# Kernel tuning notes

Measured on AMD Instinct MI355X. Metric: run time of the kernel, lower is better.

The kernel has to match this reference:

```python
import jax, jax.numpy as jnp
import numpy as np

N = 512 * 512
E = N * 8


def setup_inputs() -> dict:
    key = jax.random.key(0)
    ks = jax.random.split(key, 20)
    inp = {
        "x": jax.random.normal(ks[0], (N, 4), dtype=jnp.float32),
        "edge_src": jax.random.randint(ks[1], (E,), 0, N, dtype=jnp.int32),
        "edge_dst": jax.random.randint(ks[2], (E,), 0, N, dtype=jnp.int32),
        "grid_size": 512,
        # GCN linear weights (PyG GCNConv: lin has no bias; separate bias added after aggregation)
        "W1": jax.random.normal(ks[3], (4, 64), dtype=jnp.float32) * 0.5,
        "b1": jnp.zeros((64,), dtype=jnp.float32),
        "W2": jax.random.normal(ks[4], (64, 64), dtype=jnp.float32) * 0.125,
        "b2": jnp.zeros((64,), dtype=jnp.float32),
        "W3": jax.random.normal(ks[5], (64, 64), dtype=jnp.float32) * 0.125,
        "b3": jnp.zeros((64,), dtype=jnp.float32),
        # CNN stack (OIHW)
        "cw1": jax.random.normal(ks[6], (32, 64, 3, 3), dtype=jnp.float32) * 0.04,
        "cb1": jnp.zeros((32,), dtype=jnp.float32),
        "cw2": jax.random.normal(ks[7], (16, 32, 3, 3), dtype=jnp.float32) * 0.06,
        "cb2": jnp.zeros((16,), dtype=jnp.float32),
        "cw3": jax.random.normal(ks[8], (8, 16, 3, 3), dtype=jnp.float32) * 0.08,
        "cb3": jnp.zeros((8,), dtype=jnp.float32),
        "cw4": jax.random.normal(ks[9], (6, 8, 3, 3), dtype=jnp.float32) * 0.12,
        "cb4": jnp.zeros((6,), dtype=jnp.float32),
    }
    return inp


def _conv(x, w, b):
    # x: [1, C, H, W], w: [O, I, 3, 3]
    y = jax.lax.conv_general_dilated(x, w, (1, 1), 'SAME',
                                     dimension_numbers=('NCHW', 'OIHW', 'NCHW'))
    return y + b[None, :, None, None]


def reference(x, edge_src, edge_dst, grid_size, W1, b1, W2, b2, W3, b3,
              cw1, cb1, cw2, cb2, cw3, cb3, cw4, cb4):
    n = x.shape[0]
    loops = jnp.arange(n, dtype=edge_src.dtype)
    src = jnp.concatenate([edge_src, loops])  # message source j
    dst = jnp.concatenate([edge_dst, loops])  # aggregation target i
    ones = jnp.ones(src.shape[0], dtype=x.dtype)
    deg = jax.ops.segment_sum(ones, dst, num_segments=n)
    dinv = jnp.where(deg > 0, jax.lax.rsqrt(deg), 0.0)
    norm = (dinv[src] * dinv[dst])[:, None]  # [E+N, 1]

    def gcn(h, W, b):
        h = h @ W
        msg = h[src] * norm
        agg = jax.ops.segment_sum(msg, dst, num_segments=n)
        return agg + b

    h = jax.nn.relu(gcn(x, W1, b1))
    h = jax.nn.relu(gcn(h, W2, b2))
    h = jax.nn.relu(gcn(h, W3, b3))

    # [N, 64] -> [1, grid, grid, 64] -> [1, 64, grid, grid]
    img = h.reshape(1, grid_size, grid_size, -1).transpose(0, 3, 1, 2)
    y = jax.nn.relu(_conv(img, cw1, cb1))
    y = jax.nn.relu(_conv(y, cw2, cb2))
    y = jax.nn.relu(_conv(y, cw3, cb3))
    y = _conv(y, cw4, cb4)
    return y[0]  # [6, grid, grid]
```

## Files before the change

kernel.cpp:

```cpp
#include <hip/hip_runtime.h>

#define NN 262144
#define NE 2097152
constexpr int GS = 512;
constexpr int P  = GS * GS;
constexpr int BSTRIDE = 12288;
constexpr int PADP = 1024;

typedef __attribute__((ext_vector_type(16))) float f32x16;
typedef __attribute__((ext_vector_type(8)))  float f32x8;
typedef __attribute__((ext_vector_type(4)))  float f32x4;
typedef __attribute__((ext_vector_type(2)))  float f32x2;
typedef __attribute__((ext_vector_type(8)))  short s16x8;

__device__ __forceinline__ unsigned short f2bf(float f) {
  unsigned u = __float_as_uint(f);
  return (unsigned short)((u + 0x7FFF + ((u >> 16) & 1)) >> 16);
}
__device__ __forceinline__ float bf2f(unsigned short h) {
  return __uint_as_float((unsigned)h << 16);
}

template <int N> struct WFull;
template <> struct WFull<8> {
  f32x16 v0, v1, v2, v3; f32x8 v4;
  __device__ __forceinline__ void load(const float* p) {
    asm volatile(
      "s_load_dwordx16 %0, %5, 0x0\n\t"
      "s_load_dwordx16 %1, %5, 0x40\n\t"
      "s_load_dwordx16 %2, %5, 0x80\n\t"
      "s_load_dwordx16 %3, %5, 0xc0\n\t"
      "s_load_dwordx8  %4, %5, 0x100\n\t"
      "s_waitcnt lgkmcnt(0)"
      : "=&s"(v0), "=&s"(v1), "=&s"(v2), "=&s"(v3), "=&s"(v4)
      : "s"(p));
  }
  __device__ __forceinline__ float get(int i) const {
    return i < 16 ? v0[i] : i < 32 ? v1[i - 16] : i < 48 ? v2[i - 32]
         : i < 64 ? v3[i - 48] : v4[i - 64];
  }
};
template <> struct WFull<6> {
  f32x16 v0, v1, v2; f32x4 v3; f32x2 v4;
  __device__ __forceinline__ void load(const float* p) {
    asm volatile(
      "s_load_dwordx16 %0, %5, 0x0\n\t"
      "s_load_dwordx16 %1, %5, 0x40\n\t"
      "s_load_dwordx16 %2, %5, 0x80\n\t"
      "s_load_dwordx4  %3, %5, 0xc0\n\t"
      "s_load_dwordx2  %4, %5, 0xd0\n\t"
      "s_waitcnt lgkmcnt(0)"
      : "=&s"(v0), "=&s"(v1), "=&s"(v2), "=&s"(v3), "=&s"(v4)
      : "s"(p));
  }
  __device__ __forceinline__ float get(int i) const {
    return i < 16 ? v0[i] : i < 32 ? v1[i - 16] : i < 48 ? v2[i - 32]
         : i < 52 ? v3[i - 48] : v4[i - 52];
  }
};

__global__ __launch_bounds__(256) void k_bhist(const int4* __restrict__ dst,
                                               int* __restrict__ gb) {
  __shared__ int lc[256];
  int t = threadIdx.x;
  lc[t] = 0;
  __syncthreads();
  int base = blockIdx.x * 1024;
#pragma unroll
  for (int q = 0; q < 4; ++q) {
    int4 d = dst[base + q * 256 + t];
    atomicAdd(&lc[d.x >> 10], 1); atomicAdd(&lc[d.y >> 10], 1);
    atomicAdd(&lc[d.z >> 10], 1); atomicAdd(&lc[d.w >> 10], 1);
  }
  __syncthreads();
  atomicAdd(&gb[t], lc[t]);
}

__global__ __launch_bounds__(256) void k_bscan(const int* __restrict__ gb,
                                               int* __restrict__ bbase,
                                               int* __restrict__ bcur) {
  __shared__ int sd[256];
  int t = threadIdx.x;
  sd[t] = gb[t];
  __syncthreads();
  for (int off = 1; off < 256; off <<= 1) {
    int v = (t >= off) ? sd[t - off] : 0;
    __syncthreads();
    sd[t] += v;
    __syncthreads();
  }
  int ex = (t == 0) ? 0 : sd[t - 1];
  bbase[t] = ex;
  bcur[t]  = ex;
  if (t == 255) bbase[256] = sd[255];
}

__global__ __launch_bounds__(256) void k_bin(const int4* __restrict__ src4,
                                             const int4* __restrict__ dst4,
                                             int* __restrict__ bcur,
                                             unsigned* __restrict__ pairs) {
  __shared__ int lcnt[256], lofs[256], lcur[256];
  __shared__ unsigned lp[4096];
  int t = threadIdx.x;
  lcnt[t] = 0;
  __syncthreads();
  int base = blockIdx.x * 1024;
  int4 dreg[4], sreg[4];
#pragma unroll
  for (int q = 0; q < 4; ++q) {
    dreg[q] = dst4[base + q * 256 + t];
    sreg[q] = src4[base + q * 256 + t];
  }
#pragma unroll
  for (int q = 0; q < 4; ++q) {
    atomicAdd(&lcnt[dreg[q].x >> 10], 1); atomicAdd(&lcnt[dreg[q].y >> 10], 1);
    atomicAdd(&lcnt[dreg[q].z >> 10], 1); atomicAdd(&lcnt[dreg[q].w >> 10], 1);
  }
  __syncthreads();
  int c = lcnt[t];
  lofs[t] = c;
  __syncthreads();
  for (int off = 1; off < 256; off <<= 1) {
    int v = (t >= off) ? lofs[t - off] : 0;
    __syncthreads();
    lofs[t] += v;
    __syncthreads();
  }
  int myofs = lofs[t] - c;
  lcur[t] = myofs;
  int gb = atomicAdd(&bcur[t], c);
  __syncthreads();
#pragma unroll
  for (int q = 0; q < 4; ++q) {
    int d[4] = {dreg[q].x, dreg[q].y, dreg[q].z, dreg[q].w};
    int s[4] = {sreg[q].x, sreg[q].y, sreg[q].z, sreg[q].w};
#pragma unroll
    for (int j = 0; j < 4; ++j) {
      int pos = atomicAdd(&lcur[d[j] >> 10], 1);
      lp[pos] = ((unsigned)(d[j] & 1023) << 18) | (unsigned)s[j];
    }
  }
  __syncthreads();
  for (int k = 0; k < c; ++k) pairs[gb + k] = lp[myofs + k];
}

__global__ __launch_bounds__(256) void k_bsort(const unsigned* __restrict__ pairs,
                                               const int* __restrict__ bbase,
                                               int* __restrict__ ssrc,
                                               int* __restrict__ offs,
                                               int* __restrict__ dgr,
                                               float* __restrict__ dinv) {
  __shared__ int cnt[1024], ofs[1024], sblk[256];
  int b = blockIdx.x, t = threadIdx.x;
  int s0 = bbase[b], n = bbase[b + 1] - s0;
  int gbase = b * BSTRIDE;
  for (int i = t; i < 1024; i += 256) cnt[i] = 0;
  __syncthreads();
  for (int i = t; i < n; i += 256) {
    unsigned p = pairs[s0 + i];
    atomicAdd(&cnt[p >> 18], 1);
  }
  __syncthreads();
  int l4 = t * 4;
  int c0 = cnt[l4], c1 = cnt[l4 + 1], c2 = cnt[l4 + 2], c3 = cnt[l4 + 3];
  int a0 = (c0 + 3) & ~3, a1 = (c1 + 3) & ~3, a2 = (c2 + 3) & ~3, a3 = (c3 + 3) & ~3;
  int sum = a0 + a1 + a2 + a3;
  sblk[t] = sum;
  __syncthreads();
  for (int off = 1; off < 256; off <<= 1) {
    int v = (t >= off) ? sblk[t - off] : 0;
    __syncthreads();
    sblk[t] += v;
    __syncthreads();
  }
  int ex = sblk[t] - sum;
  int o0 = gbase + ex, o1 = o0 + a0, o2 = o1 + a1, o3 = o2 + a2;
  ofs[l4] = o0; ofs[l4 + 1] = o1; ofs[l4 + 2] = o2; ofs[l4 + 3] = o3;
  int node = b * 1024 + l4;
  *(int4*)&offs[node] = make_int4(o0, o1, o2, o3);
  *(int4*)&dgr[node]  = make_int4(c0, c1, c2, c3);
  *(float4*)&dinv[node] = make_float4(rsqrtf((float)(c0 + 1)),
                                      rsqrtf((float)(c1 + 1)),
                                      rsqrtf((float)(c2 + 1)),
                                      rsqrtf((float)(c3 + 1)));
  for (int p = c0; p < a0; ++p) ssrc[o0 + p] = NN;
  for (int p = c1; p < a1; ++p) ssrc[o1 + p] = NN;
  for (int p = c2; p < a2; ++p) ssrc[o2 + p] = NN;
  for (int p = c3; p < a3; ++p) ssrc[o3 + p] = NN;
  __syncthreads();
  for (int i = t; i < n; i += 256) {
    unsigned p = pairs[s0 + i];
    int pos = atomicAdd(&ofs[p >> 18], 1);
    ssrc[pos] = (int)(p & 0x3FFFFu);
  }
}

__global__ void k_zrows(float* hA, float* hB, float* xs) {
  int t = threadIdx.x;
  if (t < 64) hA[(size_t)NN * 64 + t] = 0.f;
  else if (t < 128) hB[(size_t)NN * 64 + (t - 64)] = 0.f;
  else if (t < 132) xs[(size_t)NN * 4 + (t - 128)] = 0.f;
}

__global__ __launch_bounds__(256) void k_xscale(const float4* __restrict__ x,
                                                const float* __restrict__ dinv,
                                                float4* __restrict__ xs) {
  int i = blockIdx.x * 256 + threadIdx.x;
  float4 v = x[i];
  float d = dinv[i];
  xs[i] = make_float4(v.x * d, v.y * d, v.z * d, v.w * d);
}

__global__ __launch_bounds__(256) void k_agg4(const float4* __restrict__ xs,
                                              const float* __restrict__ dinv,
                                              const int* __restrict__ offs,
                                              const int* __restrict__ dgr,
                                              const int4* __restrict__ ssrc4,
                                              float4* __restrict__ out) {
  for (int i = blockIdx.x * 256 + threadIdx.x; i < NN; i += gridDim.x * 256) {
    float di = dinv[i];
    int k4 = offs[i] >> 2, deg = dgr[i];
    float4 acc = xs[i];
    int t4n = (deg + 3) >> 2;
    int4 s4 = ssrc4[k4];
    for (int t4 = 0; t4 < t4n; ++t4) {
      int4 nx = ssrc4[k4 + t4 + 1];
      float4 v0 = xs[s4.x], v1 = xs[s4.y], v2 = xs[s4.z], v3 = xs[s4.w];
      acc.x += v0.x + v1.x + v2.x + v3.x;
      acc.y += v0.y + v1.y + v2.y + v3.y;
      acc.z += v0.z + v1.z + v2.z + v3.z;
      acc.w += v0.w + v1.w + v2.w + v3.w;
      s4 = nx;
    }
    out[i] = make_float4(acc.x * di, acc.y * di, acc.z * di, acc.w * di);
  }
}

__global__ __launch_bounds__(256) void k_matmul4(const float* __restrict__ h,
                                                 const float* __restrict__ W,
                                                 const float* __restrict__ bias,
                                                 const float* __restrict__ dinv,
                                                 float* __restrict__ out) {
  int lane = threadIdx.x & 63;
  int wv   = threadIdx.x >> 6;
  float w0 = W[lane], w1 = W[64 + lane], w2 = W[128 + lane], w3 = W[192 + lane];
  float bl = bias[lane];
  for (int node = blockIdx.x * 4 + wv; node < NN; node += gridDim.x * 4) {
    float4 hv = *(const float4*)(h + (size_t)node * 4);
    float dn = dinv[node];
    float acc = fmaf(hv.x, w0, fmaf(hv.y, w1, fmaf(hv.z, w2, fmaf(hv.w, w3, bl))));
    out[(size_t)node * 64 + lane] = fmaxf(acc, 0.f) * dn;
  }
}

template <bool SCALE_OUT, bool BF16OUT>
__global__ __launch_bounds__(256) void k_aggW(const float* __restrict__ h,
                                              const float* __restrict__ dinv,
                                              const int* __restrict__ offs,
                                              const int* __restrict__ dgr,
                                              const int4* __restrict__ ssrc4,
                                              const float* __restrict__ W,
                                              const float* __restrict__ bias,
                                              float* __restrict__ out,
                                              unsigned short* __restrict__ xhi,
                                              unsigned short* __restrict__ xlo) {
  __shared__ float g[16][64];
  const float4* h4 = (const float4*)h;
  int lane = threadIdx.x & 63;
  int wv   = threadIdx.x >> 6;
  int sub  = lane >> 4;
  int fl   = lane & 15;
  float wreg[64];
#pragma unroll
  for (int k = 0; k < 64; ++k) wreg[k] = W[(size_t)k * 64 + lane];
  float bl = bias[lane];

  for (int i0 = (blockIdx.x * 4 + wv) * 4; i0 < NN; i0 += gridDim.x * 16) {
    int i = i0 + sub;
    float di = dinv[i];
    int k4 = offs[i] >> 2;
    int deg = dgr[i];
    int t4n = (deg + 3) >> 2;

    float4 acc  = h4[(size_t)i * 16 + fl];
    float4 accB = make_float4(0.f, 0.f, 0.f, 0.f);
    int4 sA = ssrc4[k4];
    int t4 = 0;
#pragma unroll 1
    for (; t4 + 2 <= t4n; t4 += 2) {
      int4 sB = ssrc4[k4 + t4 + 1];
      int4 nx = ssrc4[k4 + t4 + 2];
      float4 v0 = h4[(size_t)sA.x * 16 + fl];
      float4 v1 = h4[(size_t)sA.y * 16 + fl];
      float4 v2 = h4[(size_t)sA.z * 16 + fl];
      float4 v3 = h4[(size_t)sA.w * 16 + fl];
      float4 u0 = h4[(size_t)sB.x * 16 + fl];
      float4 u1 = h4[(size_t)sB.y * 16 + fl];
      float4 u2 = h4[(size_t)sB.z * 16 + fl];
      float4 u3 = h4[(size_t)sB.w * 16 + fl];
      acc.x  += v0.x + v1.x + v2.x + v3.x;
      acc.y  += v0.y + v1.y + v2.y + v3.y;
      acc.z  += v0.z + v1.z + v2.z + v3.z;
      acc.w  += v0.w + v1.w + v2.w + v3.w;
      accB.x += u0.x + u1.x + u2.x + u3.x;
      accB.y += u0.y + u1.y + u2.y + u3.y;
      accB.z += u0.z + u1.z + u2.z + u3.z;
      accB.w += u0.w + u1.w + u2.w + u3.w;
      sA = nx;
    }
    if (t4 < t4n) {
      float4 v0 = h4[(size_t)sA.x * 16 + fl];
      float4 v1 = h4[(size_t)sA.y * 16 + fl];
      float4 v2 = h4[(size_t)sA.z * 16 + fl];
      float4 v3 = h4[(size_t)sA.w * 16 + fl];
      acc.x += v0.x + v1.x + v2.x + v3.x;
      acc.y += v0.y + v1.y + v2.y + v3.y;
      acc.z += v0.z + v1.z + v2.z + v3.z;
      acc.w += v0.w + v1.w + v2.w + v3.w;
    }
    acc.x += accB.x; acc.y += accB.y; acc.z += accB.z; acc.w += accB.w;

    float4 sacc = make_float4(acc.x * di, acc.y * di, acc.z * di, acc.w * di);
    int row = wv * 4 + sub;
    *(float4*)&g[row][fl * 4] = sacc;
    asm volatile("s_waitcnt lgkmcnt(0)" ::: "memory");

#pragma unroll
    for (int n = 0; n < 4; ++n) {
      const float4* gp = (const float4*)&g[wv * 4 + n][0];
      float o = bl;
#pragma unroll
      for (int q = 0; q < 16; ++q) {
        float4 gv = gp[q];
        o = fmaf(gv.x, wreg[q * 4 + 0], o);
        o = fmaf(gv.y, wreg[q * 4 + 1], o);
        o = fmaf(gv.z, wreg[q * 4 + 2], o);
        o = fmaf(gv.w, wreg[q * 4 + 3], o);
      }
      float val = fmaxf(o, 0.f);
      if constexpr (SCALE_OUT) val *= dinv[i0 + n];
      if constexpr (BF16OUT) {
        size_t b = (size_t)(PADP + i0 + n) * 64 + lane;
        unsigned short hh = f2bf(val);
        xhi[b] = hh;
        xlo[b] = f2bf(val - bf2f(hh));
      } else {
        out[(size_t)(i0 + n) * 64 + lane] = val;
      }
    }
  }
}

__global__ __launch_bounds__(256) void k_wrepm(const float* __restrict__ w,
                                               unsigned short* __restrict__ whim,
                                               unsigned short* __restrict__ wlom) {
  int idx = blockIdx.x * 256 + threadIdx.x;
  if (idx >= 9 * 2 * 2 * 512) return;
  int i  = idx & 7;
  int l  = (idx >> 3) & 63;
  int nf = (idx >> 9) & 1;
  int ks = (idx >> 10) & 1;
  int t  = idx >> 11;
  int o = nf * 16 + (l & 15);
  int c = ks * 32 + (l >> 4) * 8 + i;
  float v = w[(o * 64 + c) * 9 + t];
  unsigned short h = f2bf(v);
  whim[idx] = h;
  wlom[idx] = f2bf(v - bf2f(h));
}

__global__ __launch_bounds__(256) void k_conv1m(const unsigned short* __restrict__ xhi,
                                                const unsigned short* __restrict__ xlo,
                                                const unsigned short* __restrict__ whim,
                                                const unsigned short* __restrict__ wlom,
                                                const float* __restrict__ cb,
                                                float* __restrict__ outp) {
  constexpr int PXS  = 80;
  constexpr int ROWB = 66 * PXS;
  constexpr int HALF = 6 * ROWB;
  __shared__ __align__(16) unsigned char smem[2 * HALF];

  int tid  = threadIdx.x;
  int lane = tid & 63, wv = tid >> 6;
  int sx = blockIdx.x & 7, gy = blockIdx.x >> 3;
  int x0 = sx * 64, y0 = gy * 4;
  int lm = lane & 15, lc = lane >> 4;

  f32x4 acc[4][2];
#pragma unroll
  for (int mf = 0; mf < 4; ++mf)
#pragma unroll
    for (int nf = 0; nf < 2; ++nf) acc[mf][nf] = (f32x4){0.f, 0.f, 0.f, 0.f};

#pragma unroll 1
  for (int ks = 0; ks < 2; ++ks) {
    if (ks) __syncthreads();
#pragma unroll 1
    for (int it = 0; it < 13; ++it) {
      int idx = it * 256 + tid;
      if (idx < 3168) {
        int arr = idx >= 1584;
        int rem = arr ? idx - 1584 : idx;
        int chunk = rem & 3;
        int pxr = rem >> 2;
        int r = pxr / 66, px = pxr - r * 66;
        int xx = x0 - 1 + px;
        uint4 v = make_uint4(0u, 0u, 0u, 0u);
        if (xx >= 0 && xx < GS) {
          size_t p = (size_t)(PADP + (y0 - 1 + r) * GS + xx);
          const unsigned short* src = arr ? xlo : xhi;
          v = *(const uint4*)((const unsigned char*)src + p * 128 + ks * 64 + chunk * 16);
        }
        *(uint4*)(smem + arr * HALF + r * ROWB + px * PXS + chunk * 16) = v;
      }
    }
    __syncthreads();
#pragma unroll 1
    for (int t = 0; t < 9; ++t) {
      int ky = t / 3, kx = t % 3;
      const unsigned short* wb = whim + (size_t)(((t * 2 + ks) * 2) * 64 + lane) * 8;
      const unsigned short* wl = wlom + (size_t)(((t * 2 + ks) * 2) * 64 + lane) * 8;
      s16x8 bh0 = *(const s16x8*)(wb);
      s16x8 bh1 = *(const s16x8*)(wb + 512);
      s16x8 bl0 = *(const s16x8*)(wl);
      s16x8 bl1 = *(const s16x8*)(wl + 512);
      int r = wv + ky;
#pragma unroll
      for (int mf = 0; mf < 4; ++mf) {
        int px = mf * 16 + lm + kx;
        const unsigned char* ap = smem + r * ROWB + px * PXS + lc * 16;
        s16x8 ah = *(const s16x8*)(ap);
        s16x8 al = *(const s16x8*)(ap + HALF);
        acc[mf][0] = __builtin_amdgcn_mfma_f32_16x16x32_bf16(ah, bh0, acc[mf][0], 0, 0, 0);
        acc[mf][0] = __builtin_amdgcn_mfma_f32_16x16x32_bf16(ah, bl0, acc[mf][0], 0, 0, 0);
        acc[mf][0] = __builtin_amdgcn_mfma_f32_16x16x32_bf16(al, bh0, acc[mf][0], 0, 0, 0);
        acc[mf][1] = __builtin_amdgcn_mfma_f32_16x16x32_bf16(ah, bh1, acc[mf][1], 0, 0, 0);
        acc[mf][1] = __builtin_amdgcn_mfma_f32_16x16x32_bf16(ah, bl1, acc[mf][1], 0, 0, 0);
        acc[mf][1] = __builtin_amdgcn_mfma_f32_16x16x32_bf16(al, bh1, acc[mf][1], 0, 0, 0);
      }
    }
  }
  __syncthreads();

  float* lds = (float*)smem;
#pragma unroll
  for (int mf = 0; mf < 4; ++mf)
#pragma unroll
    for (int nf = 0; nf < 2; ++nf)
#pragma unroll
      for (int r = 0; r < 4; ++r)
        lds[((wv * 64 + mf * 16 + lc * 4 + r) * 33) + nf * 16 + lm] = acc[mf][nf][r];
  asm volatile("s_waitcnt lgkmcnt(0)" ::: "memory");

  size_t ob = (size_t)(y0 + wv) * GS + x0 + lane;
#pragma unroll
  for (int o = 0; o < 32; ++o) {
    float v = lds[((wv * 64 + lane) * 33) + o] + cb[o];
    outp[(size_t)o * P + ob] = fmaxf(v, 0.f);
  }
}

template <int CIN, int COUT, int COUTB>
__global__ __launch_bounds__(256) void k_wrep(const float* __restrict__ w,
                                              float* __restrict__ wr) {
  int i = blockIdx.x * 256 + threadIdx.x;
  if (i >= CIN * 9 * COUT) return;
  int ol = i % COUTB;
  int t  = (i / COUTB) % 9;
  int c  = (i / (COUTB * 9)) % CIN;
  int g  = i / (COUTB * 9 * CIN);
  wr[i] = w[(((g * COUTB + ol) * CIN) + c) * 9 + t];
}

template <int CIN, int COUTB, bool RELU>
__global__ __launch_bounds__(256) void k_conv(const float* __restrict__ in,
                                              const float* __restrict__ wrep,
                                              const float* __restrict__ cb,
                                              float* __restrict__ out) {
  int tx = threadIdx.x;
  int ty = threadIdx.y;
  int g  = blockIdx.z;
  int x0 = (blockIdx.x * 64 + tx) * 2;
  int y  = blockIdx.y * 4 + ty;

  float acc0[COUTB], acc1[COUTB];
#pragma unroll
  for (int o = 0; o < COUTB; ++o) { acc0[o] = 0.f; acc1[o] = 0.f; }

  bool xlo = x0 > 0;
  bool xhi = x0 < GS - 2;
  int rok[3], yoff[3];
#pragma unroll
  for (int r = 0; r < 3; ++r) {
    int yy = y + r - 1;
    rok[r] = (yy >= 0) && (yy < GS);
    int yc = yy < 0 ? 0 : (yy > GS - 1 ? GS - 1 : yy);
    yoff[r] = yc * GS;
  }
  const float* wg = wrep + (size_t)g * CIN * 9 * COUTB;

  WFull<COUTB> w;
#pragma unroll 1
  for (int c = 0; c < CIN; ++c) {
    float iv[3][4];
#pragma unroll
    for (int r = 0; r < 3; ++r) {
      const float* ip = in + (size_t)c * P + yoff[r] + x0;
      if (rok[r]) {
        float2 m = *(const float2*)ip;
        iv[r][1] = m.x; iv[r][2] = m.y;
        iv[r][0] = xlo ? ip[-1] : 0.f;
        iv[r][3] = xhi ? ip[2]  : 0.f;
      } else {
        iv[r][0] = iv[r][1] = iv[r][2] = iv[r][3] = 0.f;
      }
    }
    w.load(wg + (size_t)c * 9 * COUTB);
#pragma unroll
    for (int t9 = 0; t9 < 9; ++t9) {
      int ky = t9 / 3, kx = t9 % 3;
      float a = iv[ky][kx], b2 = iv[ky][kx + 1];
#pragma unroll
      for (int o = 0; o < COUTB; ++o) {
        float wv = w.get(t9 * COUTB + o);
        acc0[o] = fmaf(a, wv, acc0[o]);
        acc1[o] = fmaf(b2, wv, acc1[o]);
      }
    }
  }

  size_t obase = (size_t)(g * COUTB) * P + (size_t)y * GS + x0;
#pragma unroll
  for (int o = 0; o < COUTB; ++o) {
    float bv = cb[g * COUTB + o];
    float v0 = acc0[o] + bv;
    float v1 = acc1[o] + bv;
    if (RELU) { v0 = fmaxf(v0, 0.f); v1 = fmaxf(v1, 0.f); }
    *(float2*)&out[obase + (size_t)o * P] = make_float2(v0, v1);
  }
}

extern "C" void kernel_launch(void* const* d_in, const int* in_sizes, int n_in,
                              void* d_out, int out_size, void* d_ws, size_t ws_size,
                              hipStream_t stream) {
  const float* x   = (const float*)d_in[0];
  const int*   esr = (const int*)d_in[1];
  const int*   eds = (const int*)d_in[2];
  const float* W1  = (const float*)d_in[4];
  const float* b1  = (const float*)d_in[5];
  const float* W2  = (const float*)d_in[6];
  const float* b2  = (const float*)d_in[7];
  const float* W3  = (const float*)d_in[8];
  const float* b3  = (const float*)d_in[9];
  const float* cw1 = (const float*)d_in[10];
  const float* cb1 = (const float*)d_in[11];
  const float* cw2 = (const float*)d_in[12];
  const float* cb2 = (const float*)d_in[13];
  const float* cw3 = (const float*)d_in[14];
  const float* cb3 = (const float*)d_in[15];
  const float* cw4 = (const float*)d_in[16];
  const float* cb4 = (const float*)d_in[17];
  float* out = (float*)d_out;

  char* ws = (char*)d_ws;
  const size_t MB = 1 << 20;
  const size_t KB = 1 << 10;
  const size_t XBYTES = (size_t)(P + 2 * PADP) * 64 * 2;
  unsigned*        pairs = (unsigned*)(ws);
  float*           xs    = (float*)(ws);
  float*           hA    = (float*)(ws);
  unsigned short*  xhi   = (unsigned short*)(ws);
  unsigned short*  xlo   = (unsigned short*)(ws + XBYTES);
  float*           cA    = (float*)(ws);
  float*           xagg  = (float*)(ws + 65 * MB);
  float*           hB    = (float*)(ws + 65 * MB);
  float*           cB    = (float*)(ws + 65 * MB);
  int*             ssrc  = (int*)(ws + 130 * MB);
  float*           dinv  = (float*)(ws + 142 * MB + 8 * KB);
  int*             dgr   = (int*)(ws + 143 * MB + 16 * KB);
  int*             offs  = (int*)(ws + 144 * MB + 24 * KB);
  int*             gb    = (int*)(ws + 145 * MB + 32 * KB);
  int*             bbase = (int*)(ws + 145 * MB + 36 * KB);
  int*             bcur  = (int*)(ws + 145 * MB + 40 * KB);
  unsigned short*  whim  = (unsigned short*)(ws + 145 * MB + 48 * KB);
  unsigned short*  wlom  = (unsigned short*)(ws + 145 * MB + 88 * KB);
  float*           wr2   = (float*)(ws + 145 * MB + 128 * KB);
  float*           wr3   = wr2 + 32 * 9 * 16;
  float*           wr4   = wr3 + 16 * 9 * 8;

  k_wrepm<<<72, 256, 0, stream>>>(cw1, whim, wlom);
  k_wrep<32, 16, 8><<<(32 * 9 * 16 + 255) / 256, 256, 0, stream>>>(cw2, wr2);
  k_wrep<16,  8, 8><<<(16 * 9 *  8 + 255) / 256, 256, 0, stream>>>(cw3, wr3);
  k_wrep< 8,  6, 6><<<( 8 * 9 *  6 + 255) / 256, 256, 0, stream>>>(cw4, wr4);

  hipMemsetAsync(gb, 0, 256 * sizeof(int), stream);
  k_bhist<<<512, 256, 0, stream>>>((const int4*)eds, gb);
  k_bscan<<<1, 256, 0, stream>>>(gb, bbase, bcur);
  k_bin<<<512, 256, 0, stream>>>((const int4*)esr, (const int4*)eds, bcur, pairs);
  k_bsort<<<256, 256, 0, stream>>>(pairs, bbase, ssrc, offs, dgr, dinv);

  k_zrows<<<1, 256, 0, stream>>>(hA, hB, xs);
  k_xscale<<<NN / 256, 256, 0, stream>>>((const float4*)x, dinv, (float4*)xs);
  k_agg4<<<1024, 256, 0, stream>>>((const float4*)xs, dinv, offs, dgr,
                                   (const int4*)ssrc, (float4*)xagg);
  k_matmul4<<<2048, 256, 0, stream>>>(xagg, W1, b1, dinv, hA);
  k_aggW<true, false><<<2048, 256, 0, stream>>>(hA, dinv, offs, dgr,
                                                (const int4*)ssrc, W2, b2, hB,
                                                nullptr, nullptr);
  const size_t PADB = (size_t)PADP * 64 * 2;
  hipMemsetAsync((char*)xhi, 0, PADB, stream);
  hipMemsetAsync((char*)xhi + (size_t)(PADP + P) * 128, 0, PADB, stream);
  hipMemsetAsync((char*)xlo, 0, PADB, stream);
  hipMemsetAsync((char*)xlo + (size_t)(PADP + P) * 128, 0, PADB, stream);
  k_aggW<false, true><<<2048, 256, 0, stream>>>(hB, dinv, offs, dgr,
                                                (const int4*)ssrc, W3, b3, hB,
                                                xhi, xlo);

  k_conv1m<<<1024, 256, 0, stream>>>(xhi, xlo, whim, wlom, cb1, cB);
  k_conv<32, 8, true ><<<dim3(4, 128, 2), dim3(64, 4), 0, stream>>>(cB, wr2, cb2, cA);
  k_conv<16, 8, true ><<<dim3(4, 128, 1), dim3(64, 4), 0, stream>>>(cA, wr3, cb3, cB);
  k_conv< 8, 6, false><<<dim3(4, 128, 1), dim3(64, 4), 0, stream>>>(cB, wr4, cb4, out);
}
```

Baseline: 427.2 us.

## Run conv2 on MFMA with split-bf16 NHWC output from conv1

Conv1 now writes its ReLU output as pixel-major hi/lo bf16 pairs instead of planar fp32. A new MFMA-based conv2 kernel reads this layout through LDS tiles and uses three bf16 MFMAs per tile to approximate fp32 accuracy, replacing the scalar fp32 conv for the 32→16 layer. This aims to cut the FP32 ALU cost of conv2 and the fp32 intermediate traffic. In exchange it adds padding memsets and relies on split-bf16 precision.

```diff
diff --git a/kernel.cpp b/kernel.cpp
--- a/kernel.cpp
+++ b/kernel.cpp
@@ -6,6 +6,7 @@
 constexpr int P  = GS * GS;
 constexpr int BSTRIDE = 12288;
 constexpr int PADP = 1024;
+constexpr int PADP2 = 1024;
 
 typedef __attribute__((ext_vector_type(16))) float f32x16;
 typedef __attribute__((ext_vector_type(8)))  float f32x8;
@@ -369,12 +370,29 @@
   wlom[idx] = f2bf(v - bf2f(h));
 }
 
+__global__ __launch_bounds__(256) void k_wrepm2(const float* __restrict__ w,
+                                                unsigned short* __restrict__ whim,
+                                                unsigned short* __restrict__ wlom) {
+  int idx = blockIdx.x * 256 + threadIdx.x;
+  if (idx >= 9 * 512) return;
+  int i = idx & 7;
+  int l = (idx >> 3) & 63;
+  int t = idx >> 9;
+  int o = l & 15;
+  int c = (l >> 4) * 8 + i;
+  float v = w[(o * 32 + c) * 9 + t];
+  unsigned short h = f2bf(v);
+  whim[idx] = h;
+  wlom[idx] = f2bf(v - bf2f(h));
+}
+
 __global__ __launch_bounds__(256) void k_conv1m(const unsigned short* __restrict__ xhi,
                                                 const unsigned short* __restrict__ xlo,
                                                 const unsigned short* __restrict__ whim,
                                                 const unsigned short* __restrict__ wlom,
                                                 const float* __restrict__ cb,
-                                                float* __restrict__ outp) {
+                                                unsigned short* __restrict__ y2hi,
+                                                unsigned short* __restrict__ y2lo) {
   constexpr int PXS  = 80;
   constexpr int ROWB = 66 * PXS;
   constexpr int HALF = 6 * ROWB;
@@ -452,10 +470,98 @@
         lds[((wv * 64 + mf * 16 + lc * 4 + r) * 33) + nf * 16 + lm] = acc[mf][nf][r];
   asm volatile("s_waitcnt lgkmcnt(0)" ::: "memory");
 
+  size_t pp = (size_t)PADP2 + (size_t)(y0 + wv) * GS + x0 + lane;
+  unsigned uh[16], ul[16];
+#pragma unroll
+  for (int o2 = 0; o2 < 16; ++o2) {
+    float v0 = fmaxf(lds[(wv * 64 + lane) * 33 + 2 * o2]     + cb[2 * o2],     0.f);
+    float v1 = fmaxf(lds[(wv * 64 + lane) * 33 + 2 * o2 + 1] + cb[2 * o2 + 1], 0.f);
+    unsigned short h0 = f2bf(v0), h1 = f2bf(v1);
+    unsigned short l0 = f2bf(v0 - bf2f(h0)), l1 = f2bf(v1 - bf2f(h1));
+    uh[o2] = (unsigned)h0 | ((unsigned)h1 << 16);
+    ul[o2] = (unsigned)l0 | ((unsigned)l1 << 16);
+  }
+  uint4* dh = (uint4*)(y2hi + pp * 32);
+  uint4* dl = (uint4*)(y2lo + pp * 32);
+#pragma unroll
+  for (int q = 0; q < 4; ++q) {
+    dh[q] = make_uint4(uh[q * 4], uh[q * 4 + 1], uh[q * 4 + 2], uh[q * 4 + 3]);
+    dl[q] = make_uint4(ul[q * 4], ul[q * 4 + 1], ul[q * 4 + 2], ul[q * 4 + 3]);
+  }
+}
+
+__global__ __launch_bounds__(256) void k_conv2m(const unsigned short* __restrict__ y2hi,
+                                                const unsigned short* __restrict__ y2lo,
+                                                const unsigned short* __restrict__ whim,
+                                                const unsigned short* __restrict__ wlom,
+                                                const float* __restrict__ cb,
+                                                float* __restrict__ outp) {
+  constexpr int PXS  = 80;
+  constexpr int ROWB = 66 * PXS;
+  constexpr int HALF = 6 * ROWB;
+  __shared__ __align__(16) unsigned char smem[2 * HALF];
+
+  int tid  = threadIdx.x;
+  int lane = tid & 63, wv = tid >> 6;
+  int sx = blockIdx.x & 7, gy = blockIdx.x >> 3;
+  int x0 = sx * 64, y0 = gy * 4;
+  int lm = lane & 15, lc = lane >> 4;
+
+  f32x4 acc[4];
+#pragma unroll
+  for (int mf = 0; mf < 4; ++mf) acc[mf] = (f32x4){0.f, 0.f, 0.f, 0.f};
+
+#pragma unroll 1
+  for (int it = 0; it < 13; ++it) {
+    int idx = it * 256 + tid;
+    if (idx < 3168) {
+      int arr = idx >= 1584;
+      int rem = arr ? idx - 1584 : idx;
+      int chunk = rem & 3;
+      int pxr = rem >> 2;
+      int r = pxr / 66, px = pxr - r * 66;
+      int xx = x0 - 1 + px;
+      uint4 v = make_uint4(0u, 0u, 0u, 0u);
+      if (xx >= 0 && xx < GS) {
+        size_t p = (size_t)(PADP2 + (y0 - 1 + r) * GS + xx);
+        const unsigned short* src = arr ? y2lo : y2hi;
+        v = *(const uint4*)((const unsigned char*)src + p * 64 + chunk * 16);
+      }
+      *(uint4*)(smem + arr * HALF + r * ROWB + px * PXS + chunk * 16) = v;
+    }
+  }
+  __syncthreads();
+#pragma unroll 1
+  for (int t = 0; t < 9; ++t) {
+    int ky = t / 3, kx = t % 3;
+    s16x8 bh = *(const s16x8*)(whim + ((size_t)t * 64 + lane) * 8);
+    s16x8 bl = *(const s16x8*)(wlom + ((size_t)t * 64 + lane) * 8);
+    int r = wv + ky;
+#pragma unroll
+    for (int mf = 0; mf < 4; ++mf) {
+      int px = mf * 16 + lm + kx;
+      const unsigned char* ap = smem + r * ROWB + px * PXS + lc * 16;
+      s16x8 ah = *(const s16x8*)(ap);
+      s16x8 al = *(const s16x8*)(ap + HALF);
+      acc[mf] = __builtin_amdgcn_mfma_f32_16x16x32_bf16(ah, bh, acc[mf], 0, 0, 0);
+      acc[mf] = __builtin_amdgcn_mfma_f32_16x16x32_bf16(ah, bl, acc[mf], 0, 0, 0);
+      acc[mf] = __builtin_amdgcn_mfma_f32_16x16x32_bf16(al, bh, acc[mf], 0, 0, 0);
+    }
+  }
+  __syncthreads();
+
+  float* lds = (float*)smem;
+#pragma unroll
+  for (int mf = 0; mf < 4; ++mf)
+#pragma unroll
+    for (int r = 0; r < 4; ++r)
+      lds[((wv * 64 + mf * 16 + lc * 4 + r) * 17) + lm] = acc[mf][r];
+  asm volatile("s_waitcnt lgkmcnt(0)" ::: "memory");
+
   size_t ob = (size_t)(y0 + wv) * GS + x0 + lane;
 #pragma unroll
-  for (int o = 0; o < 32; ++o) {
-    float v = lds[((wv * 64 + lane) * 33) + o] + cb[o];
+  for (int o = 0; o < 16; ++o) {
+    float v = lds[((wv * 64 + lane) * 17) + o] + cb[o];
     outp[(size_t)o * P + ob] = fmaxf(v, 0.f);
   }
 }
@@ -574,7 +680,9 @@
   float*           cA    = (float*)(ws);
   float*           xagg  = (float*)(ws + 65 * MB);
   float*           hB    = (float*)(ws + 65 * MB);
-  float*           cB    = (float*)(ws + 65 * MB);
+  unsigned short*  y2hi  = (unsigned short*)(ws + 65 * MB);
+  unsigned short*  y2lo  = (unsigned short*)(ws + 83 * MB);
+  float*           cB8   = (float*)(ws + 101 * MB);
   int*             ssrc  = (int*)(ws + 130 * MB);
   float*           dinv  = (float*)(ws + 142 * MB + 8 * KB);
   int*             dgr   = (int*)(ws + 143 * MB + 16 * KB);
@@ -584,12 +692,13 @@
   int*             bcur  = (int*)(ws + 145 * MB + 40 * KB);
   unsigned short*  whim  = (unsigned short*)(ws + 145 * MB + 48 * KB);
   unsigned short*  wlom  = (unsigned short*)(ws + 145 * MB + 88 * KB);
-  float*           wr2   = (float*)(ws + 145 * MB + 128 * KB);
-  float*           wr3   = wr2 + 32 * 9 * 16;
+  float*           wr3   = (float*)(ws + 145 * MB + 128 * KB);
   float*           wr4   = wr3 + 16 * 9 * 8;
+  unsigned short*  whim2 = (unsigned short*)(ws + 145 * MB + 160 * KB);
+  unsigned short*  wlom2 = (unsigned short*)(ws + 145 * MB + 176 * KB);
 
   k_wrepm<<<72, 256, 0, stream>>>(cw1, whim, wlom);
-  k_wrep<32, 16, 8><<<(32 * 9 * 16 + 255) / 256, 256, 0, stream>>>(cw2, wr2);
+  k_wrepm2<<<18, 256, 0, stream>>>(cw2, whim2, wlom2);
   k_wrep<16,  8, 8><<<(16 * 9 *  8 + 255) / 256, 256, 0, stream>>>(cw3, wr3);
   k_wrep< 8,  6, 6><<<( 8 * 9 *  6 + 255) / 256, 256, 0, stream>>>(cw4, wr4);
 
@@ -616,8 +725,13 @@
                                                 (const int4*)ssrc, W3, b3, hB,
                                                 xhi, xlo);
 
-  k_conv1m<<<1024, 256, 0, stream>>>(xhi, xlo, whim, wlom, cb1, cB);
-  k_conv<32, 8, true ><<<dim3(4, 128, 2), dim3(64, 4), 0, stream>>>(cB, wr2, cb2, cA);
-  k_conv<16, 8, true ><<<dim3(4, 128, 1), dim3(64, 4), 0, stream>>>(cA, wr3, cb3, cB);
-  k_conv< 8, 6, false><<<dim3(4, 128, 1), dim3(64, 4), 0, stream>>>(cB, wr4, cb4, out);
-}
+  const size_t PADB2 = (size_t)PADP2 * 32 * 2;
+  hipMemsetAsync((char*)y2hi, 0, PADB2, stream);
+  hipMemsetAsync((char*)y2hi + (size_t)(PADP2 + P) * 64, 0, PADB2, stream);
+  hipMemsetAsync((char*)y2lo, 0, PADB2, stream);
+  hipMemsetAsync((char*)y2lo + (size_t)(PADP2 + P) * 64, 0, PADB2, stream);
+  k_conv1m<<<1024, 256, 0, stream>>>(xhi, xlo, whim, wlom, cb1, y2hi, y2lo);
+  k_conv2m<<<1024, 256, 0, stream>>>(y2hi, y2lo, whim2, wlom2, cb2, cA);
+  k_conv<16, 8, true ><<<dim3(4, 128, 1), dim3(64, 4), 0, stream>>>(cA, wr3, cb3, cB8);
+  k_conv< 8, 6, false><<<dim3(4, 128, 1), dim3(64, 4), 0, stream>>>(cB8, wr4, cb4, out);
+}
```

Measured after the change: 424.5 us (median of 2 runs). About the same (-0.6%).
